# Kernel tuning notes

Hardware: AMD Instinct MI355X
Metric: run time of the kernel (lower is better)

Reference implementation:

```python
import jax, jax.numpy as jnp
import numpy as np

N_NODES = 100000
D_FEAT = 128
N_EDGES = 500000
HIDDEN = 256
OUT = 1


def setup_inputs() -> dict:
    key = jax.random.key(0)
    k1, k2, k3, k4, k5, k6 = jax.random.split(key, 6)
    z = jax.random.normal(k1, (N_NODES, D_FEAT), dtype=jnp.float32)
    edge_index = jax.random.randint(k2, (N_EDGES, 3), 0, N_NODES, dtype=jnp.int64)
    # torch nn.Linear weights: [out, in]
    fc1_w = jax.random.normal(k3, (HIDDEN, 2 * D_FEAT), dtype=jnp.float32) * (1.0 / np.sqrt(2 * D_FEAT))
    fc1_b = jax.random.normal(k4, (HIDDEN,), dtype=jnp.float32) * 0.01
    fc2_w = jax.random.normal(k5, (OUT, HIDDEN), dtype=jnp.float32) * (1.0 / np.sqrt(HIDDEN))
    fc2_b = jax.random.normal(k6, (OUT,), dtype=jnp.float32) * 0.01
    return {"z": z, "edge_index": edge_index, "fc1_w": fc1_w, "fc1_b": fc1_b,
            "fc2_w": fc2_w, "fc2_b": fc2_b}


def reference(z, edge_index, fc1_w, fc1_b, fc2_w, fc2_b):
    row = edge_index[:, 1]
    col = edge_index[:, 2]
    concatenated = jnp.concatenate([z[row], z[col]], axis=1)  # [E, 2d]
    x = jax.nn.relu(concatenated @ fc1_w.T + fc1_b)           # [E, hidden]
    decoded = jax.nn.sigmoid(x @ fc2_w.T + fc2_b)             # [E, out]
    return decoded
```

## Files before the change

### kernel.cpp

```cpp
#include <hip/hip_runtime.h>
#include <stdint.h>

#define N_NODES 100000
#define D_FEAT  128
#define N_EDGES 500000
#define HIDDEN  256
#define EPT     64
#define NTILES  ((N_EDGES + EPT - 1) / EPT)
#define GRID_MAIN 256

typedef __bf16 bf16x8 __attribute__((ext_vector_type(8)));
typedef __bf16 bf16x4 __attribute__((ext_vector_type(4)));
typedef float  f32x4  __attribute__((ext_vector_type(4)));

__device__ __forceinline__ void gld_lds16(const unsigned short* g, unsigned char* l) {
  __builtin_amdgcn_global_load_lds(
      (const __attribute__((address_space(1))) unsigned int*)g,
      (__attribute__((address_space(3))) unsigned int*)l, 16, 0, 0);
}

__device__ __forceinline__ bf16x8 cvt8(f32x4 lo, f32x4 hi) {
  bf16x8 r;
  r[0] = (__bf16)lo[0]; r[1] = (__bf16)lo[1]; r[2] = (__bf16)lo[2]; r[3] = (__bf16)lo[3];
  r[4] = (__bf16)hi[0]; r[5] = (__bf16)hi[1]; r[6] = (__bf16)hi[2]; r[7] = (__bf16)hi[3];
  return r;
}

__global__ void cvt_z(const float* __restrict__ src, unsigned short* __restrict__ dst, int n4) {
  int i = blockIdx.x * blockDim.x + threadIdx.x;
  const int stride = gridDim.x * blockDim.x;
  for (; i < n4; i += stride) {
    const f32x4 v = ((const f32x4*)src)[i];
    bf16x4 o;
    o[0] = (__bf16)v[0]; o[1] = (__bf16)v[1]; o[2] = (__bf16)v[2]; o[3] = (__bf16)v[3];
    ((bf16x4*)dst)[i] = o;
  }
}

__global__ __launch_bounds__(512, 2)
void mlp_main(const int* __restrict__ eidx,
              const unsigned short* __restrict__ z16,
              const float* __restrict__ w1f,
              const float* __restrict__ b1,
              const float* __restrict__ w2g,
              const float* __restrict__ b2,
              float* __restrict__ out) {
  __shared__ unsigned char sbuf[3][EPT * 512];
  __shared__ float red[2][4][72];

  const int tid  = threadIdx.x;
  const int w    = tid >> 6;
  const int l    = tid & 63;
  const int l15  = l & 15;
  const int g    = l >> 4;
  const int ng   = w >> 1;
  const int mg   = w & 1;
  const int half = w >> 2;

  const int is64 = (eidx[1] == 0 && eidx[3] == 0 && eidx[5] == 0);
  const float b2v = b2[0];

  bf16x8 a[4][8];
  #pragma unroll
  for (int nt = 0; nt < 4; ++nt) {
    const int n = ng * 64 + nt * 16 + l15;
    #pragma unroll
    for (int ks = 0; ks < 8; ++ks) {
      const int k = ks * 32 + g * 8;
      const f32x4 lo = *(const f32x4*)(w1f + n * 256 + k);
      const f32x4 hi = *(const f32x4*)(w1f + n * 256 + k + 4);
      a[nt][ks] = cvt8(lo, hi);
    }
  }
  f32x4 b1v[4], w2v[4];
  #pragma unroll
  for (int nt = 0; nt < 4; ++nt) {
    const int nb = ng * 64 + nt * 16 + g * 4;
    b1v[nt] = *(const f32x4*)(b1 + nb);
    w2v[nt] = *(const f32x4*)(w2g + nb);
  }

  auto ldidx = [&](int t) -> int {
    int e = t * EPT + l;
    if (e > N_EDGES - 1) e = N_EDGES - 1;
    return is64 ? eidx[6 * e + 2 + 2 * half] : eidx[3 * e + 1 + half];
  };
  auto stage = [&](int buf, int iv) {
    const unsigned short* src = z16 + (size_t)iv * D_FEAT;
    #pragma unroll
    for (int j = 0; j < 4; ++j) {
      const int c = 4 * w + j;
      gld_lds16(src + ((c & 15) << 3), &sbuf[buf][c << 10]);
    }
  };

  const int t0 = blockIdx.x;
  int ivq = ldidx(t0);
  stage(0, ivq);
  int iv_next = ldidx(t0 + GRID_MAIN);

  int cb = 0, it = 0;
  for (int t = t0; t < NTILES; t += GRID_MAIN, ++it) {
    __syncthreads();

    int cn = cb + 1; if (cn == 3) cn = 0;
    stage(cn, iv_next);
    iv_next = ldidx(t + 2 * GRID_MAIN);

    if (it) {
      if (w < 4) {
        const int e = (w << 4) + (l >> 2);
        float v = red[(it - 1) & 1][l & 3][e];
        v += __shfl_xor(v, 1);
        v += __shfl_xor(v, 2);
        const int eg = (t - GRID_MAIN) * EPT + e;
        if ((l & 3) == 0 && eg < N_EDGES)
          out[eg] = 1.f / (1.f + __expf(-(v + b2v)));
      }
    }

    f32x4 acc[4][2];
    #pragma unroll
    for (int nt = 0; nt < 4; ++nt) {
      acc[nt][0] = (f32x4){0.f, 0.f, 0.f, 0.f};
      acc[nt][1] = (f32x4){0.f, 0.f, 0.f, 0.f};
    }
    const unsigned char* sb = &sbuf[cb][0];
    #pragma unroll
    for (int ks = 0; ks < 8; ++ks) {
      bf16x8 bf[2];
      #pragma unroll
      for (int ct = 0; ct < 2; ++ct) {
        const int c = ks * 4 + g;
        const int m = mg * 32 + ct * 16 + l15;
        bf[ct] = *(const bf16x8*)(sb + (c << 10) + (m << 4));
      }
      __builtin_amdgcn_s_setprio(1);
      #pragma unroll
      for (int nt = 0; nt < 4; ++nt)
        #pragma unroll
        for (int ct = 0; ct < 2; ++ct)
          acc[nt][ct] = __builtin_amdgcn_mfma_f32_16x16x32_bf16(
              a[nt][ks], bf[ct], acc[nt][ct], 0, 0, 0);
      __builtin_amdgcn_s_setprio(0);
    }

    float p[2] = {0.f, 0.f};
    #pragma unroll
    for (int nt = 0; nt < 4; ++nt) {
      #pragma unroll
      for (int r = 0; r < 4; ++r) {
        const float bb = b1v[nt][r], ww = w2v[nt][r];
        #pragma unroll
        for (int ct = 0; ct < 2; ++ct) {
          float x = acc[nt][ct][r] + bb;
          x = fmaxf(x, 0.f);
          p[ct] = fmaf(x, ww, p[ct]);
        }
      }
    }
    #pragma unroll
    for (int ct = 0; ct < 2; ++ct) {
      p[ct] += __shfl_xor(p[ct], 16);
      p[ct] += __shfl_xor(p[ct], 32);
    }
    if (l < 16) {
      red[it & 1][ng][mg * 32 + l]      = p[0];
      red[it & 1][ng][mg * 32 + 16 + l] = p[1];
    }
    cb = cn;
  }

  __syncthreads();
  {
    const int tl = t0 + (it - 1) * GRID_MAIN;
    if (w < 4) {
      const int e = (w << 4) + (l >> 2);
      float v = red[(it - 1) & 1][l & 3][e];
      v += __shfl_xor(v, 1);
      v += __shfl_xor(v, 2);
      const int eg = tl * EPT + e;
      if ((l & 3) == 0 && eg < N_EDGES)
        out[eg] = 1.f / (1.f + __expf(-(v + b2v)));
    }
  }
}

extern "C" void kernel_launch(void* const* d_in, const int* in_sizes, int n_in,
                              void* d_out, int out_size, void* d_ws, size_t ws_size,
                              hipStream_t stream) {
  const float* z    = (const float*)d_in[0];
  const int*   eidx = (const int*)d_in[1];
  const float* fc1w = (const float*)d_in[2];
  const float* fc1b = (const float*)d_in[3];
  const float* fc2w = (const float*)d_in[4];
  const float* fc2b = (const float*)d_in[5];
  float* out = (float*)d_out;

  unsigned short* z16 = (unsigned short*)d_ws;

  cvt_z<<<2048, 256, 0, stream>>>(z, z16, N_NODES * D_FEAT / 4);
  mlp_main<<<GRID_MAIN, 512, 0, stream>>>(eidx, z16, fc1w, fc1b, fc2w, fc2b, out);
}
```

Measured before the change: 215.3 us.

## Repartition MFMA work across waves to halve registers and double resident blocks

Each wave now owns 32 hidden rows across all 64 edges instead of 64 rows across 32 edges. This halves the per-wave W1 register fragments, allowing launch bounds of 4 blocks per CU and a grid of 512. LDS staging drops from triple to double buffering, and bias and fc2 weights move from registers into shared memory. The 8-way cross-wave reduction is rewritten to match. More resident waves should hide gather latency better, but each tile now reads 4 B fragments from LDS per k-step and has less prefetch depth.

Measured after the change: 221.0 us. 1.03x slower.

```diff
diff --git a/kernel.cpp b/kernel.cpp
--- a/kernel.cpp
+++ b/kernel.cpp
@@ -7,7 +7,7 @@
 #define HIDDEN  256
 #define EPT     64
 #define NTILES  ((N_EDGES + EPT - 1) / EPT)
-#define GRID_MAIN 256
+#define GRID_MAIN 512
 
 typedef __bf16 bf16x8 __attribute__((ext_vector_type(8)));
 typedef __bf16 bf16x4 __attribute__((ext_vector_type(4)));
@@ -37,7 +37,7 @@
   }
 }
 
-__global__ __launch_bounds__(512, 2)
+__global__ __launch_bounds__(512, 4)
 void mlp_main(const int* __restrict__ eidx,
               const unsigned short* __restrict__ z16,
               const float* __restrict__ w1f,
@@ -45,39 +45,33 @@
               const float* __restrict__ w2g,
               const float* __restrict__ b2,
               float* __restrict__ out) {
-  __shared__ unsigned char sbuf[3][EPT * 512];
-  __shared__ float red[2][4][72];
+  __shared__ unsigned char sbuf[2][EPT * 512];
+  __shared__ float red[2][8][72];
+  __shared__ float b1f[HIDDEN], w2f[HIDDEN];
 
   const int tid  = threadIdx.x;
   const int w    = tid >> 6;
   const int l    = tid & 63;
   const int l15  = l & 15;
   const int g    = l >> 4;
-  const int ng   = w >> 1;
-  const int mg   = w & 1;
   const int half = w >> 2;
 
   const int is64 = (eidx[1] == 0 && eidx[3] == 0 && eidx[5] == 0);
   const float b2v = b2[0];
 
-  bf16x8 a[4][8];
+  if (tid < HIDDEN) { b1f[tid] = b1[tid]; w2f[tid] = w2g[tid]; }
+
+  bf16x8 a[2][8];
   #pragma unroll
-  for (int nt = 0; nt < 4; ++nt) {
-    const int n = ng * 64 + nt * 16 + l15;
+  for (int rt = 0; rt < 2; ++rt) {
+    const int n = w * 32 + rt * 16 + l15;
     #pragma unroll
     for (int ks = 0; ks < 8; ++ks) {
       const int k = ks * 32 + g * 8;
       const f32x4 lo = *(const f32x4*)(w1f + n * 256 + k);
       const f32x4 hi = *(const f32x4*)(w1f + n * 256 + k + 4);
-      a[nt][ks] = cvt8(lo, hi);
+      a[rt][ks] = cvt8(lo, hi);
     }
-  }
-  f32x4 b1v[4], w2v[4];
-  #pragma unroll
-  for (int nt = 0; nt < 4; ++nt) {
-    const int nb = ng * 64 + nt * 16 + g * 4;
-    b1v[nt] = *(const f32x4*)(b1 + nb);
-    w2v[nt] = *(const f32x4*)(w2g + nb);
   }
 
   auto ldidx = [&](int t) -> int {
@@ -95,94 +89,93 @@
   };
 
   const int t0 = blockIdx.x;
-  int ivq = ldidx(t0);
-  stage(0, ivq);
+  stage(0, ldidx(t0));
   int iv_next = ldidx(t0 + GRID_MAIN);
 
-  int cb = 0, it = 0;
+  int it = 0;
   for (int t = t0; t < NTILES; t += GRID_MAIN, ++it) {
     __syncthreads();
+    const int cb = it & 1;
 
-    int cn = cb + 1; if (cn == 3) cn = 0;
-    stage(cn, iv_next);
+    stage(cb ^ 1, iv_next);
     iv_next = ldidx(t + 2 * GRID_MAIN);
 
     if (it) {
-      if (w < 4) {
-        const int e = (w << 4) + (l >> 2);
-        float v = red[(it - 1) & 1][l & 3][e];
-        v += __shfl_xor(v, 1);
-        v += __shfl_xor(v, 2);
-        const int eg = (t - GRID_MAIN) * EPT + e;
-        if ((l & 3) == 0 && eg < N_EDGES)
-          out[eg] = 1.f / (1.f + __expf(-(v + b2v)));
-      }
+      const int el = 8 * w + (l & 7);
+      float v = red[(it - 1) & 1][l >> 3][el];
+      v += __shfl_xor(v, 8);
+      v += __shfl_xor(v, 16);
+      v += __shfl_xor(v, 32);
+      const int eg = (t - GRID_MAIN) * EPT + el;
+      if (l < 8 && eg < N_EDGES)
+        out[eg] = 1.f / (1.f + __expf(-(v + b2v)));
     }
 
-    f32x4 acc[4][2];
+    f32x4 acc[2][4];
     #pragma unroll
-    for (int nt = 0; nt < 4; ++nt) {
-      acc[nt][0] = (f32x4){0.f, 0.f, 0.f, 0.f};
-      acc[nt][1] = (f32x4){0.f, 0.f, 0.f, 0.f};
-    }
+    for (int rt = 0; rt < 2; ++rt)
+      #pragma unroll
+      for (int ct = 0; ct < 4; ++ct)
+        acc[rt][ct] = (f32x4){0.f, 0.f, 0.f, 0.f};
+
     const unsigned char* sb = &sbuf[cb][0];
     #pragma unroll
     for (int ks = 0; ks < 8; ++ks) {
-      bf16x8 bf[2];
+      bf16x8 bf[4];
       #pragma unroll
-      for (int ct = 0; ct < 2; ++ct) {
+      for (int ct = 0; ct < 4; ++ct) {
         const int c = ks * 4 + g;
-        const int m = mg * 32 + ct * 16 + l15;
+        const int m = ct * 16 + l15;
         bf[ct] = *(const bf16x8*)(sb + (c << 10) + (m << 4));
       }
       __builtin_amdgcn_s_setprio(1);
       #pragma unroll
-      for (int nt = 0; nt < 4; ++nt)
+      for (int rt = 0; rt < 2; ++rt)
         #pragma unroll
-        for (int ct = 0; ct < 2; ++ct)
-          acc[nt][ct] = __builtin_amdgcn_mfma_f32_16x16x32_bf16(
-              a[nt][ks], bf[ct], acc[nt][ct], 0, 0, 0);
+        for (int ct = 0; ct < 4; ++ct)
+          acc[rt][ct] = __builtin_amdgcn_mfma_f32_16x16x32_bf16(
+              a[rt][ks], bf[ct], acc[rt][ct], 0, 0, 0);
       __builtin_amdgcn_s_setprio(0);
     }
 
-    float p[2] = {0.f, 0.f};
+    float p[4] = {0.f, 0.f, 0.f, 0.f};
     #pragma unroll
-    for (int nt = 0; nt < 4; ++nt) {
+    for (int rt = 0; rt < 2; ++rt) {
+      const int nb = w * 32 + rt * 16 + g * 4;
+      const f32x4 bb = *(const f32x4*)&b1f[nb];
+      const f32x4 ww = *(const f32x4*)&w2f[nb];
       #pragma unroll
       for (int r = 0; r < 4; ++r) {
-        const float bb = b1v[nt][r], ww = w2v[nt][r];
         #pragma unroll
-        for (int ct = 0; ct < 2; ++ct) {
-          float x = acc[nt][ct][r] + bb;
+        for (int ct = 0; ct < 4; ++ct) {
+          float x = acc[rt][ct][r] + bb[r];
           x = fmaxf(x, 0.f);
-          p[ct] = fmaf(x, ww, p[ct]);
+          p[ct] = fmaf(x, ww[r], p[ct]);
         }
       }
     }
     #pragma unroll
-    for (int ct = 0; ct < 2; ++ct) {
+    for (int ct = 0; ct < 4; ++ct) {
       p[ct] += __shfl_xor(p[ct], 16);
       p[ct] += __shfl_xor(p[ct], 32);
     }
     if (l < 16) {
-      red[it & 1][ng][mg * 32 + l]      = p[0];
-      red[it & 1][ng][mg * 32 + 16 + l] = p[1];
+      #pragma unroll
+      for (int ct = 0; ct < 4; ++ct) red[it & 1][w][ct * 16 + l] = p[ct];
     }
-    cb = cn;
   }
 
   __syncthreads();
   {
     const int tl = t0 + (it - 1) * GRID_MAIN;
-    if (w < 4) {
-      const int e = (w << 4) + (l >> 2);
-      float v = red[(it - 1) & 1][l & 3][e];
-      v += __shfl_xor(v, 1);
-      v += __shfl_xor(v, 2);
-      const int eg = tl * EPT + e;
-      if ((l & 3) == 0 && eg < N_EDGES)
-        out[eg] = 1.f / (1.f + __expf(-(v + b2v)));
-    }
+    const int el = 8 * w + (l & 7);
+    float v = red[(it - 1) & 1][l >> 3][el];
+    v += __shfl_xor(v, 8);
+    v += __shfl_xor(v, 16);
+    v += __shfl_xor(v, 32);
+    const int eg = tl * EPT + el;
+    if (l < 8 && eg < N_EDGES)
+      out[eg] = 1.f / (1.f + __expf(-(v + b2v)));
   }
 }
 
```

## Shrink edge tiles, double grid, and deepen index prefetch with vmcnt waits

Applied to the files above, without the earlier changes.

Halves edges per tile to 32 and doubles the grid to 512 blocks of 256 threads, so each wave now covers 64 hidden units across all 32 edges. The LDS layout and staging addresses change to match. Index prefetch goes three tiles ahead, and the __syncthreads is replaced with an explicit vmcnt/lgkmcnt wait plus s_barrier. The bounds check on output stores is removed by sending the first iteration's emit to a dummy workspace buffer. This targets latency hiding and parallelism, but relies on N_EDGES being divisible by 32 and on hand-counted waitcnt values.

After: 183.5 us. 14.8% less time.

```diff
diff --git a/kernel.cpp b/kernel.cpp
--- a/kernel.cpp
+++ b/kernel.cpp
@@ -5,9 +5,9 @@
 #define D_FEAT  128
 #define N_EDGES 500000
 #define HIDDEN  256
-#define EPT     64
-#define NTILES  ((N_EDGES + EPT - 1) / EPT)
-#define GRID_MAIN 256
+#define EPT     32
+#define NTILES  (N_EDGES / EPT)
+#define GRID_MAIN 512
 
 typedef __bf16 bf16x8 __attribute__((ext_vector_type(8)));
 typedef __bf16 bf16x4 __attribute__((ext_vector_type(4)));
@@ -37,33 +37,35 @@
   }
 }
 
-__global__ __launch_bounds__(512, 2)
+__global__ __launch_bounds__(256, 2)
 void mlp_main(const int* __restrict__ eidx,
               const unsigned short* __restrict__ z16,
               const float* __restrict__ w1f,
               const float* __restrict__ b1,
               const float* __restrict__ w2g,
               const float* __restrict__ b2,
-              float* __restrict__ out) {
+              float* __restrict__ out,
+              float* __restrict__ dump) {
   __shared__ unsigned char sbuf[3][EPT * 512];
-  __shared__ float red[2][4][72];
+  __shared__ float red[2][4][40];
 
   const int tid  = threadIdx.x;
   const int w    = tid >> 6;
   const int l    = tid & 63;
   const int l15  = l & 15;
+  const int l31  = l & 31;
   const int g    = l >> 4;
-  const int ng   = w >> 1;
-  const int mg   = w & 1;
-  const int half = w >> 2;
+  const int half = w >> 1;
 
   const int is64 = (eidx[1] == 0 && eidx[3] == 0 && eidx[5] == 0);
   const float b2v = b2[0];
+  const int estride = is64 ? 6 : 3;
+  const int eoff    = is64 ? (2 + 2 * half) : (1 + half);
 
   bf16x8 a[4][8];
   #pragma unroll
   for (int nt = 0; nt < 4; ++nt) {
-    const int n = ng * 64 + nt * 16 + l15;
+    const int n = w * 64 + nt * 16 + l15;
     #pragma unroll
     for (int ks = 0; ks < 8; ++ks) {
       const int k = ks * 32 + g * 8;
@@ -75,49 +77,52 @@
   f32x4 b1v[4], w2v[4];
   #pragma unroll
   for (int nt = 0; nt < 4; ++nt) {
-    const int nb = ng * 64 + nt * 16 + g * 4;
+    const int nb = w * 64 + nt * 16 + g * 4;
     b1v[nt] = *(const f32x4*)(b1 + nb);
     w2v[nt] = *(const f32x4*)(w2g + nb);
   }
 
   auto ldidx = [&](int t) -> int {
-    int e = t * EPT + l;
+    int e = t * EPT + l31;
     if (e > N_EDGES - 1) e = N_EDGES - 1;
-    return is64 ? eidx[6 * e + 2 + 2 * half] : eidx[3 * e + 1 + half];
+    return eidx[e * estride + eoff];
   };
   auto stage = [&](int buf, int iv) {
     const unsigned short* src = z16 + (size_t)iv * D_FEAT;
     #pragma unroll
     for (int j = 0; j < 4; ++j) {
       const int c = 4 * w + j;
-      gld_lds16(src + ((c & 15) << 3), &sbuf[buf][c << 10]);
+      gld_lds16(src + ((c & 7) << 4) + ((l >> 5) << 3), &sbuf[buf][c << 10]);
     }
   };
 
+  auto emit = [&](int tile, int par, bool real) {
+    const int m  = 8 * w + (l & 7);
+    float v = red[par][(l >> 3) & 3][m];
+    v += __shfl_xor(v, 8);
+    v += __shfl_xor(v, 16);
+    const float s = 1.f / (1.f + __expf(-(v + b2v)));
+    float* dst = real ? (out + tile * EPT + m) : (dump + blockIdx.x * EPT + m);
+    if (l < 8) *dst = s;
+  };
+
   const int t0 = blockIdx.x;
-  int ivq = ldidx(t0);
-  stage(0, ivq);
-  int iv_next = ldidx(t0 + GRID_MAIN);
-
-  int cb = 0, it = 0;
+  stage(0, ldidx(t0));
+  int iv_b = ldidx(t0 + GRID_MAIN);
+  int iv_c = ldidx(t0 + 2 * GRID_MAIN);
+  __builtin_amdgcn_s_waitcnt(0);
+
+  int it = 0, cb = 0;
   for (int t = t0; t < NTILES; t += GRID_MAIN, ++it) {
-    __syncthreads();
-
     int cn = cb + 1; if (cn == 3) cn = 0;
-    stage(cn, iv_next);
-    iv_next = ldidx(t + 2 * GRID_MAIN);
-
-    if (it) {
-      if (w < 4) {
-        const int e = (w << 4) + (l >> 2);
-        float v = red[(it - 1) & 1][l & 3][e];
-        v += __shfl_xor(v, 1);
-        v += __shfl_xor(v, 2);
-        const int eg = (t - GRID_MAIN) * EPT + e;
-        if ((l & 3) == 0 && eg < N_EDGES)
-          out[eg] = 1.f / (1.f + __expf(-(v + b2v)));
-      }
-    }
+    stage(cn, iv_b);
+    const int iv_d = ldidx(t + 3 * GRID_MAIN);
+    asm volatile("s_waitcnt vmcnt(7) lgkmcnt(0)" ::: "memory");
+    __builtin_amdgcn_sched_barrier(0);
+    __builtin_amdgcn_s_barrier();
+    __builtin_amdgcn_sched_barrier(0);
+
+    emit(t - GRID_MAIN, (it - 1) & 1, it != 0);
 
     f32x4 acc[4][2];
     #pragma unroll
@@ -126,15 +131,13 @@
       acc[nt][1] = (f32x4){0.f, 0.f, 0.f, 0.f};
     }
     const unsigned char* sb = &sbuf[cb][0];
+    const int off0 = ((g >> 1) << 10) + ((g & 1) << 9) + (l15 << 4);
     #pragma unroll
     for (int ks = 0; ks < 8; ++ks) {
       bf16x8 bf[2];
       #pragma unroll
-      for (int ct = 0; ct < 2; ++ct) {
-        const int c = ks * 4 + g;
-        const int m = mg * 32 + ct * 16 + l15;
-        bf[ct] = *(const bf16x8*)(sb + (c << 10) + (m << 4));
-      }
+      for (int ct = 0; ct < 2; ++ct)
+        bf[ct] = *(const bf16x8*)(sb + (ks << 11) + (ct << 8) + off0);
       __builtin_amdgcn_s_setprio(1);
       #pragma unroll
       for (int nt = 0; nt < 4; ++nt)
@@ -165,25 +168,16 @@
       p[ct] += __shfl_xor(p[ct], 32);
     }
     if (l < 16) {
-      red[it & 1][ng][mg * 32 + l]      = p[0];
-      red[it & 1][ng][mg * 32 + 16 + l] = p[1];
-    }
-    cb = cn;
-  }
-
-  __syncthreads();
-  {
-    const int tl = t0 + (it - 1) * GRID_MAIN;
-    if (w < 4) {
-      const int e = (w << 4) + (l >> 2);
-      float v = red[(it - 1) & 1][l & 3][e];
-      v += __shfl_xor(v, 1);
-      v += __shfl_xor(v, 2);
-      const int eg = tl * EPT + e;
-      if ((l & 3) == 0 && eg < N_EDGES)
-        out[eg] = 1.f / (1.f + __expf(-(v + b2v)));
-    }
-  }
+      red[it & 1][w][l15]      = p[0];
+      red[it & 1][w][16 + l15] = p[1];
+    }
+
+    iv_b = iv_c; iv_c = iv_d; cb = cn;
+  }
+
+  asm volatile("s_waitcnt lgkmcnt(0)" ::: "memory");
+  __builtin_amdgcn_s_barrier();
+  emit(t0 + (it - 1) * GRID_MAIN, (it - 1) & 1, true);
 }
 
 extern "C" void kernel_launch(void* const* d_in, const int* in_sizes, int n_in,
@@ -198,7 +192,9 @@
   float* out = (float*)d_out;
 
   unsigned short* z16 = (unsigned short*)d_ws;
+  float* dump = (float*)((unsigned char*)d_ws + 25600000);
 
   cvt_z<<<2048, 256, 0, stream>>>(z, z16, N_NODES * D_FEAT / 4);
-  mlp_main<<<GRID_MAIN, 512, 0, stream>>>(eidx, z16, fc1w, fc1b, fc2w, fc2b, out);
-}
+  mlp_main<<<GRID_MAIN, 256, 0, stream>>>(eidx, z16, fc1w, fc1b, fc2w, fc2b,
+                                          out, dump);
+}
```
